# Kernel tuning notes

Measured on AMD Instinct MI355X. Metric: run time of the kernel, lower is better.

The kernel has to match this reference:

```python
import jax, jax.numpy as jnp
import numpy as np

N_CLASSES = 4
ALPHA = 2.0
BIG = jnp.float32(1e9)  # stands in for +inf at non-site pixels


def _dt1d_sq(f):
    # Exact 1D squared distance transform along the last axis:
    # out[i] = min_j f[j] + (i - j)^2  (brute-force lower envelope, fully vectorized)
    n = f.shape[-1]
    i = jnp.arange(n, dtype=f.dtype)
    d2 = (i[:, None] - i[None, :]) ** 2  # [n, n]
    return jnp.min(f[..., None, :] + d2, axis=-1)


def _edt_sq(sites):
    # Exact squared Euclidean distance to the nearest True pixel (separable 2D DT).
    f = jnp.where(sites, jnp.float32(0.0), BIG)
    f = _dt1d_sq(f)                                  # pass along W
    f = jnp.swapaxes(_dt1d_sq(jnp.swapaxes(f, -1, -2)), -1, -2)  # pass along H
    return f


def _distance_field(img):
    # Mirrors HausdorffDTLoss.distance_field:
    #   fg_dist = edt(fg_mask)  (distance to nearest bg pixel, 0 on bg)
    #   bg_dist = edt(~fg_mask) (distance to nearest fg pixel, 0 on fg)
    #   field = fg_dist + bg_dist if fg_mask.any() else 0
    fg = img > 0.5                                   # [B, H, W] bool
    fg_dist = jnp.sqrt(_edt_sq(~fg))                 # dist to nearest background
    bg_dist = jnp.sqrt(_edt_sq(fg))                  # dist to nearest foreground
    any_fg = jnp.any(fg, axis=(-2, -1), keepdims=True)
    return jnp.where(any_fg, fg_dist + bg_dist, jnp.float32(0.0))


def reference(pred, target):
    # pred: [B, 4, H, W] logits; target: [B, H, W] int labels in [0, 4)
    probs = jax.nn.softmax(pred, axis=1)
    tgt = jnp.moveaxis(jax.nn.one_hot(target, N_CLASSES, dtype=probs.dtype), -1, 1)  # [B,4,H,W]
    total = jnp.float32(0.0)
    for i in range(N_CLASSES):
        p = probs[:, i]
        t = tgt[:, i]
        pred_dt = jax.lax.stop_gradient(_distance_field(p))
        target_dt = jax.lax.stop_gradient(_distance_field(t))
        pred_error = (p - t) ** 2
        distance = pred_dt ** ALPHA + target_dt ** ALPHA
        total = total + jnp.mean(pred_error * distance)
    return total / N_CLASSES


def setup_inputs() -> dict:
    key = jax.random.key(0)
    k1, k2 = jax.random.split(key)
    pred = jax.random.normal(k1, (4, 4, 256, 256), dtype=jnp.float32)
    target = jax.random.randint(k2, (4, 256, 256), 0, 4).astype(jnp.int32)
    return {"pred": pred, "target": target}
```

## Files before the change

kernel.cpp:

```cpp
#include <hip/hip_runtime.h>

#define HH 256
#define WW 256
#define NB 4
#define NC 4
#define NPIX (HH*WW)
#define NIMG (NB*NC)
#define TOTAL (NB*NC*HH*WW)
#define INF_G (1<<30)
#define PAD 257

__device__ __forceinline__ float wave_reduce(float v) {
    #pragma unroll
    for (int off = 32; off > 0; off >>= 1) v += __shfl_down(v, off);
    return v;
}

__device__ __forceinline__ int nearest_dist(const unsigned long long* m, int x) {
    int best = 0x7fffffff;
    #pragma unroll
    for (int w = 0; w < 4; ++w) {
        unsigned long long mm = m[w];
        if (!mm) continue;
        int rel = x - (w << 6);
        unsigned long long lmask = (rel >= 63) ? ~0ull
                                 : ((rel < 0) ? 0ull : ((2ull << (rel & 63)) - 1ull));
        unsigned long long lm = mm & lmask;
        if (lm) best = min(best, rel - (63 - __clzll(lm)));
        unsigned long long rmask = (rel <= 0) ? ~0ull
                                 : ((rel > 63) ? 0ull : (~0ull << (rel & 63)));
        unsigned long long rm = mm & rmask;
        if (rm) best = min(best, (__ffsll((long long)rm) - 1) - rel);
    }
    return best;
}

__global__ __launch_bounds__(1024) void build_masks(
        const float* __restrict__ pred, const int* __restrict__ target,
        unsigned long long* __restrict__ masks, float* __restrict__ out) {
    int bid = blockIdx.x;
    int t = threadIdx.x;
    int b = bid >> 6, rg = bid & 63;
    int x = t & 255;
    int y = (rg << 2) + (t >> 8);
    int w = x >> 6;

    if (bid == 0 && t == 0) out[0] = 0.0f;

    const float* base = pred + (((size_t)b * NC) * HH + y) * WW + x;
    float v0 = base[0 * (size_t)NPIX];
    float v1 = base[1 * (size_t)NPIX];
    float v2 = base[2 * (size_t)NPIX];
    float v3 = base[3 * (size_t)NPIX];
    float m = fmaxf(fmaxf(v0, v1), fmaxf(v2, v3));
    float e0 = expf(v0 - m), e1 = expf(v1 - m), e2 = expf(v2 - m), e3 = expf(v3 - m);
    float inv = 1.0f / (e0 + e1 + e2 + e3);
    float p[4] = { e0 * inv, e1 * inv, e2 * inv, e3 * inv };

    int tc = target[((size_t)b * HH + y) * WW + x];

    #pragma unroll
    for (int c = 0; c < 4; ++c) {
        unsigned long long bp = __ballot(p[c] > 0.5f);
        unsigned long long bt = __ballot(tc == c);
        if ((t & 63) == 0) {
            size_t mi = ((size_t)(b * NC + c)) * 2;
            masks[((mi + 0) * 4 + w) * HH + y] = bp;
            masks[((mi + 1) * 4 + w) * HH + y] = bt;
        }
    }
}

__global__ __launch_bounds__(1024) void cols_loss(const unsigned long long* __restrict__ masks,
                                                  const float* __restrict__ pred,
                                                  float* __restrict__ out) {
    int bid = blockIdx.x;
    int img = bid >> 5;
    int xbase = (bid & 31) << 3;
    int b = img >> 2, c = img & 3;
    int t = threadIdx.x;
    int lane = t & 63, wv = t >> 6;

    __shared__ unsigned long long sm[2048];
    __shared__ int hP[8 * PAD], hT[8 * PAD];
    __shared__ float pe_s[8 * PAD];
    __shared__ int sF[2][16];
    __shared__ float sred[16];

    const unsigned long long* mb = masks + (size_t)img * 2048;
    #pragma unroll
    for (int j = 0; j < 2; ++j) sm[t + 1024 * j] = mb[t + 1024 * j];
    __syncthreads();

    bool anyP = false, anyT = false;
    if (t < 256) {
        unsigned long long rp = sm[0 * HH + t] | sm[1 * HH + t] | sm[2 * HH + t] | sm[3 * HH + t];
        unsigned long long rt = sm[4 * HH + t] | sm[5 * HH + t] | sm[6 * HH + t] | sm[7 * HH + t];
        anyP = (rp != 0ull); anyT = (rt != 0ull);
    }
    unsigned long long bP = __ballot(anyP), bT = __ballot(anyT);
    if (lane == 0) { sF[0][wv] = (bP != 0ull); sF[1][wv] = (bT != 0ull); }

    #pragma unroll
    for (int j = 0; j < 2; ++j) {
        int idx = t + 1024 * j;
        int cx = idx & 7, y = idx >> 3;
        int x = xbase + cx;

        unsigned long long mp[4], mt[4];
        #pragma unroll
        for (int w = 0; w < 4; ++w) {
            mp[w] = sm[w * HH + y];
            mt[w] = sm[(4 + w) * HH + y];
        }
        int fgP = (int)((mp[x >> 6] >> (x & 63)) & 1);
        int fgT = (int)((mt[x >> 6] >> (x & 63)) & 1);

        unsigned long long sel[4];
        unsigned long long flip = fgP ? ~0ull : 0ull;
        #pragma unroll
        for (int w = 0; w < 4; ++w) sel[w] = mp[w] ^ flip;
        int dP = nearest_dist(sel, x);
        int vP = (dP > 255) ? INF_G : dP * dP;
        hP[cx * PAD + y] = vP | (fgP << 31);

        flip = fgT ? ~0ull : 0ull;
        #pragma unroll
        for (int w = 0; w < 4; ++w) sel[w] = mt[w] ^ flip;
        int dT = nearest_dist(sel, x);
        int vT = (dT > 255) ? INF_G : dT * dT;
        hT[cx * PAD + y] = vT | (fgT << 31);

        const float* basep = pred + ((size_t)b * NC) * NPIX + (size_t)y * WW + x;
        float v0 = basep[0 * (size_t)NPIX];
        float v1 = basep[1 * (size_t)NPIX];
        float v2 = basep[2 * (size_t)NPIX];
        float v3 = basep[3 * (size_t)NPIX];
        float m = fmaxf(fmaxf(v0, v1), fmaxf(v2, v3));
        float e0 = expf(v0 - m), e1 = expf(v1 - m), e2 = expf(v2 - m), e3 = expf(v3 - m);
        float inv = 1.0f / (e0 + e1 + e2 + e3);
        float pc = (c == 0) ? e0 * inv : (c == 1) ? e1 * inv : (c == 2) ? e2 * inv : e3 * inv;
        float d = pc - (float)fgT;
        pe_s[cx * PAD + y] = d * d;
    }
    __syncthreads();

    int hs1 = 0, hs3 = 0;
    #pragma unroll
    for (int i = 0; i < 16; ++i) { hs1 |= sF[0][i]; hs3 |= sF[1][i]; }

    float acc = 0.0f;
    int y = t & 255, cg2 = t >> 8;
    #pragma unroll
    for (int i = 0; i < 2; ++i) {
        int cx = cg2 * 2 + i;
        const int* hp = &hP[cx * PAD];
        const int* ht = &hT[cx * PAD];

        int selfP = hp[y];
        int msP = selfP & 0x80000000;
        int best = selfP & 0x7fffffff;
        for (int s = 1; s < HH; ++s) {
            int ss = s * s;
            if (ss >= best) break;
            int jm = y - s, jp = y + s;
            if (jm >= 0) {
                int hsv = hp[jm];
                int cand = (((hsv ^ msP) & 0x80000000) == 0) ? (hsv & 0x7fffffff) + ss : ss;
                best = min(best, cand);
            }
            if (jp < HH) {
                int hsv = hp[jp];
                int cand = (((hsv ^ msP) & 0x80000000) == 0) ? (hsv & 0x7fffffff) + ss : ss;
                best = min(best, cand);
            }
        }
        float dtP = (best >= INF_G) ? sqrtf(1.0e9f) : sqrtf((float)best);

        int selfT = ht[y];
        int msT = selfT & 0x80000000;
        best = selfT & 0x7fffffff;
        for (int s = 1; s < HH; ++s) {
            int ss = s * s;
            if (ss >= best) break;
            int jm = y - s, jp = y + s;
            if (jm >= 0) {
                int hsv = ht[jm];
                int cand = (((hsv ^ msT) & 0x80000000) == 0) ? (hsv & 0x7fffffff) + ss : ss;
                best = min(best, cand);
            }
            if (jp < HH) {
                int hsv = ht[jp];
                int cand = (((hsv ^ msT) & 0x80000000) == 0) ? (hsv & 0x7fffffff) + ss : ss;
                best = min(best, cand);
            }
        }
        float dtT = (best >= INF_G) ? sqrtf(1.0e9f) : sqrtf((float)best);

        float pd = hs1 ? dtP : 0.0f;
        float td = hs3 ? dtT : 0.0f;
        acc += pe_s[cx * PAD + y] * (pd * pd + td * td);
    }

    acc = wave_reduce(acc);
    if (lane == 0) sred[wv] = acc;
    __syncthreads();
    if (t == 0) {
        float bs = 0.0f;
        #pragma unroll
        for (int i = 0; i < 16; ++i) bs += sred[i];
        unsafeAtomicAdd(out, bs * (1.0f / (float)TOTAL));
    }
}

extern "C" void kernel_launch(void* const* d_in, const int* in_sizes, int n_in,
                              void* d_out, int out_size, void* d_ws, size_t ws_size,
                              hipStream_t stream) {
    const float* pred  = (const float*)d_in[0];
    const int* target  = (const int*)d_in[1];
    float* out = (float*)d_out;

    unsigned long long* masks = (unsigned long long*)d_ws;

    build_masks<<<NB * 64, 1024, 0, stream>>>(pred, target, masks, out);
    cols_loss<<<NIMG * 32, 1024, 0, stream>>>(masks, pred, out);
}
```

Measured before the change: 28.30 us.

## Fuse mask building into loss kernel with per-block redundant mask recomputation

Merges the two kernels into one: each block recomputes the full 256x256 softmax masks for its image in shared memory instead of reading precomputed masks from a workspace. Block count is halved and each block now handles 16 columns instead of 8. This removes a kernel launch and the global mask round-trip, but every block rereads the whole image's logits and targets, multiplying redundant global reads and exp work. A memset replaces the in-kernel zeroing of the output.

```diff
diff --git a/kernel.cpp b/kernel.cpp
--- a/kernel.cpp
+++ b/kernel.cpp
@@ -35,83 +35,71 @@
     return best;
 }
 
-__global__ __launch_bounds__(1024) void build_masks(
+__global__ __launch_bounds__(1024) void fused_all(
         const float* __restrict__ pred, const int* __restrict__ target,
-        unsigned long long* __restrict__ masks, float* __restrict__ out) {
+        float* __restrict__ out) {
     int bid = blockIdx.x;
-    int t = threadIdx.x;
-    int b = bid >> 6, rg = bid & 63;
-    int x = t & 255;
-    int y = (rg << 2) + (t >> 8);
-    int w = x >> 6;
-
-    if (bid == 0 && t == 0) out[0] = 0.0f;
-
-    const float* base = pred + (((size_t)b * NC) * HH + y) * WW + x;
-    float v0 = base[0 * (size_t)NPIX];
-    float v1 = base[1 * (size_t)NPIX];
-    float v2 = base[2 * (size_t)NPIX];
-    float v3 = base[3 * (size_t)NPIX];
-    float m = fmaxf(fmaxf(v0, v1), fmaxf(v2, v3));
-    float e0 = expf(v0 - m), e1 = expf(v1 - m), e2 = expf(v2 - m), e3 = expf(v3 - m);
-    float inv = 1.0f / (e0 + e1 + e2 + e3);
-    float p[4] = { e0 * inv, e1 * inv, e2 * inv, e3 * inv };
-
-    int tc = target[((size_t)b * HH + y) * WW + x];
-
-    #pragma unroll
-    for (int c = 0; c < 4; ++c) {
-        unsigned long long bp = __ballot(p[c] > 0.5f);
-        unsigned long long bt = __ballot(tc == c);
-        if ((t & 63) == 0) {
-            size_t mi = ((size_t)(b * NC + c)) * 2;
-            masks[((mi + 0) * 4 + w) * HH + y] = bp;
-            masks[((mi + 1) * 4 + w) * HH + y] = bt;
-        }
-    }
-}
-
-__global__ __launch_bounds__(1024) void cols_loss(const unsigned long long* __restrict__ masks,
-                                                  const float* __restrict__ pred,
-                                                  float* __restrict__ out) {
-    int bid = blockIdx.x;
-    int img = bid >> 5;
-    int xbase = (bid & 31) << 3;
+    int k8 = bid & 7, q = bid >> 3;
+    int img = (k8 << 1) + (q >> 4);
+    int xbase = (q & 15) << 4;
     int b = img >> 2, c = img & 3;
     int t = threadIdx.x;
     int lane = t & 63, wv = t >> 6;
 
-    __shared__ unsigned long long sm[2048];
-    __shared__ int hP[8 * PAD], hT[8 * PAD];
-    __shared__ float pe_s[8 * PAD];
+    __shared__ unsigned long long smP[1024], smT[1024];
+    __shared__ int hP[16 * PAD], hT[16 * PAD];
+    __shared__ float pe_s[16 * PAD];
     __shared__ int sF[2][16];
     __shared__ float sred[16];
 
-    const unsigned long long* mb = masks + (size_t)img * 2048;
-    #pragma unroll
-    for (int j = 0; j < 2; ++j) sm[t + 1024 * j] = mb[t + 1024 * j];
+    {
+        int x = t & 255;
+        int w = x >> 6;
+        int yq = t >> 8;
+        const float* pb = pred + ((size_t)b * NC) * NPIX + x;
+        const int* tb = target + (size_t)b * NPIX + x;
+        for (int j = 0; j < 64; ++j) {
+            int y = (yq << 6) + j;
+            size_t ro = (size_t)y * WW;
+            float v0 = pb[0 * (size_t)NPIX + ro];
+            float v1 = pb[1 * (size_t)NPIX + ro];
+            float v2 = pb[2 * (size_t)NPIX + ro];
+            float v3 = pb[3 * (size_t)NPIX + ro];
+            float m = fmaxf(fmaxf(v0, v1), fmaxf(v2, v3));
+            float e0 = expf(v0 - m), e1 = expf(v1 - m), e2 = expf(v2 - m), e3 = expf(v3 - m);
+            float inv = 1.0f / (e0 + e1 + e2 + e3);
+            float pc = (c == 0) ? e0 * inv : (c == 1) ? e1 * inv : (c == 2) ? e2 * inv : e3 * inv;
+            int tc = tb[ro];
+            unsigned long long bp = __ballot(pc > 0.5f);
+            unsigned long long bt = __ballot(tc == c);
+            if (lane == 0) {
+                smP[w * HH + y] = bp;
+                smT[w * HH + y] = bt;
+            }
+        }
+    }
     __syncthreads();
 
     bool anyP = false, anyT = false;
     if (t < 256) {
-        unsigned long long rp = sm[0 * HH + t] | sm[1 * HH + t] | sm[2 * HH + t] | sm[3 * HH + t];
-        unsigned long long rt = sm[4 * HH + t] | sm[5 * HH + t] | sm[6 * HH + t] | sm[7 * HH + t];
+        unsigned long long rp = smP[0 * HH + t] | smP[1 * HH + t] | smP[2 * HH + t] | smP[3 * HH + t];
+        unsigned long long rt = smT[0 * HH + t] | smT[1 * HH + t] | smT[2 * HH + t] | smT[3 * HH + t];
         anyP = (rp != 0ull); anyT = (rt != 0ull);
     }
     unsigned long long bP = __ballot(anyP), bT = __ballot(anyT);
     if (lane == 0) { sF[0][wv] = (bP != 0ull); sF[1][wv] = (bT != 0ull); }
 
     #pragma unroll
-    for (int j = 0; j < 2; ++j) {
+    for (int j = 0; j < 4; ++j) {
         int idx = t + 1024 * j;
-        int cx = idx & 7, y = idx >> 3;
+        int cx = idx & 15, y = idx >> 4;
         int x = xbase + cx;
 
         unsigned long long mp[4], mt[4];
         #pragma unroll
         for (int w = 0; w < 4; ++w) {
-            mp[w] = sm[w * HH + y];
-            mt[w] = sm[(4 + w) * HH + y];
+            mp[w] = smP[w * HH + y];
+            mt[w] = smT[w * HH + y];
         }
         int fgP = (int)((mp[x >> 6] >> (x & 63)) & 1);
         int fgT = (int)((mt[x >> 6] >> (x & 63)) & 1);
@@ -152,8 +140,8 @@
     float acc = 0.0f;
     int y = t & 255, cg2 = t >> 8;
     #pragma unroll
-    for (int i = 0; i < 2; ++i) {
-        int cx = cg2 * 2 + i;
+    for (int i = 0; i < 4; ++i) {
+        int cx = cg2 * 4 + i;
         const int* hp = &hP[cx * PAD];
         const int* ht = &hT[cx * PAD];
 
@@ -220,8 +208,6 @@
     const int* target  = (const int*)d_in[1];
     float* out = (float*)d_out;
 
-    unsigned long long* masks = (unsigned long long*)d_ws;
-
-    build_masks<<<NB * 64, 1024, 0, stream>>>(pred, target, masks, out);
-    cols_loss<<<NIMG * 32, 1024, 0, stream>>>(masks, pred, out);
-}
+    hipMemsetAsync(out, 0, sizeof(float), stream);
+    fused_all<<<NIMG * 16, 1024, 0, stream>>>(pred, target, out);
+}
```

After: 70.81 us. 2.5x slower.
